# Kernel optimization log

Hardware: AMD Instinct MI355X
Metric: run time of the kernel (lower is better)

Reference implementation:

```python
import jax, jax.numpy as jnp
import numpy as np

IMG = 640
NUM_CLASSES = 80
MAX_MATCHES = 10  # == num_gt (required by the module's one-hot loop broadcast)
ALPHA = 0.5
BETA = 6.0
EPS = 1e-05
KEPS = 1e-07  # keras backend epsilon


def _make_anchor_points():
    pts = []
    for s in (8, 16, 32):
        n = IMG // s
        xs = (jnp.arange(n, dtype=jnp.float32) + 0.5) * s
        gx, gy = jnp.meshgrid(xs, xs, indexing='xy')
        pts.append(jnp.stack([gx, gy], axis=-1).reshape(-1, 2))
    return jnp.concatenate(pts, axis=0)  # [8400, 2]


def setup_inputs() -> dict:
    key = jax.random.key(0)
    ks = jax.random.split(key, 6)
    B, A, C, G = 32, 8400, NUM_CLASSES, 10
    anchors = _make_anchor_points()                                  # [A,2]
    scores = jax.random.uniform(ks[0], (B, A, C), dtype=jnp.float32)
    # predicted boxes roughly centered on anchors
    ctr = anchors[None] + 8.0 * jax.random.normal(ks[1], (B, A, 2), dtype=jnp.float32)
    wh = 8.0 + 56.0 * jax.random.uniform(ks[2], (B, A, 2), dtype=jnp.float32)
    decode_bboxes = jnp.concatenate([ctr - wh / 2, ctr + wh / 2], axis=-1)  # [B,A,4]
    # ground-truth boxes (xyxy within image)
    gmin = jax.random.uniform(ks[3], (B, G, 2), dtype=jnp.float32) * (IMG - 170.0)
    gwh = 20.0 + 150.0 * jax.random.uniform(ks[4], (B, G, 2), dtype=jnp.float32)
    gt_bboxes = jnp.concatenate([gmin, gmin + gwh], axis=-1)         # [B,G,4]
    gt_labels = jax.random.randint(ks[5], (B, G), 0, C, dtype=jnp.int32)
    gt_mask = jnp.ones((B, G, 1), dtype=bool)
    return {"scores": scores, "decode_bboxes": decode_bboxes, "anchors": anchors,
            "gt_labels": gt_labels, "gt_bboxes": gt_bboxes, "gt_mask": gt_mask}


def compute_ciou(b1, b2):
    # b1 [B,G,1,4], b2 [B,1,A,4] -> [B,G,A]
    x1a, y1a, x2a, y2a = (b1[..., i] for i in range(4))
    x1b, y1b, x2b, y2b = (b2[..., i] for i in range(4))
    w1 = x2a - x1a
    h1 = y2a - y1a + 1e-05
    w2 = x2b - x1b
    h2 = y2b - y1b + 1e-05
    inter = (jnp.maximum(jnp.minimum(x2a, x2b) - jnp.maximum(x1a, x1b), 0.0) *
             jnp.maximum(jnp.minimum(y2a, y2b) - jnp.maximum(y1a, y1b), 0.0))
    union = w1 * h1 + w2 * h2 - inter + 1e-05
    iou = inter / (union + 1e-05)
    cw = jnp.maximum(x2a, x2b) - jnp.minimum(x1a, x1b)
    ch = jnp.maximum(y2a, y2b) - jnp.minimum(y1a, y1b)
    c2 = cw ** 2 + ch ** 2 + KEPS
    rho2 = (((x1a + x2a) - (x1b + x2b)) / 2) ** 2 + (((y1a + y2a) - (y1b + y2b)) / 2) ** 2
    v = (4.0 / np.pi ** 2) * (jnp.arctan(w2 / h2) - jnp.arctan(w1 / h1)) ** 2
    alpha = v / (v - iou + (1.0 + KEPS))
    return iou - (rho2 / c2 + v * alpha)


def reference(scores, decode_bboxes, anchors, gt_labels, gt_bboxes, gt_mask):
    B, A, C = scores.shape
    G = gt_bboxes.shape[1]
    # per-gt class score for every anchor: [B,G,A]
    idx = jnp.broadcast_to(jnp.maximum(gt_labels, 0)[:, None, :], (B, A, G))
    bbox_scores = jnp.take_along_axis(scores, idx, axis=-1)          # [B,A,G]
    bbox_scores = jnp.transpose(bbox_scores, (0, 2, 1))              # [B,G,A]
    overlaps = compute_ciou(gt_bboxes[:, :, None, :], decode_bboxes[:, None, :, :])  # [B,G,A]
    align = jnp.power(bbox_scores, ALPHA) * jnp.power(overlaps, BETA)
    align = jnp.where(gt_mask, align, 0.0)
    # anchor center strictly inside gt box: [B,G,A]
    in_box = jnp.all((gt_bboxes[:, :, None, :2] < anchors) &
                     (gt_bboxes[:, :, None, 2:] > anchors), axis=-1)
    align = jnp.where(in_box, align, 0.0)
    cand_vals, cand_idxs = jax.lax.top_k(align, MAX_MATCHES)         # [B,G,K]
    cand_idxs = jnp.where(cand_vals > 0, cand_idxs, -1)
    # faithful to original loop: sum_k one_hot(cand_idxs[:, k], A)  -> sum over axis 1
    matched = jax.nn.one_hot(cand_idxs, A, dtype=overlaps.dtype).sum(axis=1)  # [B,K,A]==[B,G,A]
    overlaps = overlaps * matched
    gt_match = jnp.argmax(overlaps, axis=1).astype(jnp.int32)        # [B,A]
    match_mask = jnp.max(overlaps, axis=1) > 0                       # [B,A]
    bbox_labels = jnp.take_along_axis(
        gt_bboxes, jnp.broadcast_to(gt_match[:, :, None], (B, A, 4)), axis=1)  # [B,A,4]
    bbox_labels = jnp.where(match_mask[:, :, None], bbox_labels, -1.0)
    class_labels = jnp.take_along_axis(gt_labels, gt_match, axis=1)  # [B,A]
    class_labels = jnp.where(match_mask, class_labels, -1)
    class_labels = jax.nn.one_hot(class_labels, C, dtype=scores.dtype)  # [B,A,C]
    align = align * matched
    max_align = jnp.max(align, axis=-1, keepdims=True)               # [B,G,1]
    max_overlap = jnp.max(overlaps, axis=-1, keepdims=True)          # [B,G,1]
    norm_align = jnp.max(align * max_overlap / (max_align + EPS), axis=-2)  # [B,A]
    class_labels = class_labels * norm_align[:, :, None]
    fg_mask = (gt_match > -1).astype(jnp.float32)                    # [B,A]
    return (jax.lax.stop_gradient(bbox_labels.reshape(-1, A, 4)),
            jax.lax.stop_gradient(class_labels),
            jax.lax.stop_gradient(fg_mask))
```

## Files before the change

kernel.cpp:

```cpp
#include <hip/hip_runtime.h>
#include <math.h>

#define A_TOT 8400
#define NGT 10
#define NCLS 80
#define KTOP 10
#define NB_BATCH 32
#define CAP 1024

typedef unsigned int u32;
typedef unsigned long long u64;

struct GtP {
    float x1, y1, x2, y2;
    float area1;
    float at1;
    float sx, sy;
    int lab;
    int rawlab;
};

__device__ __forceinline__ void compute_pair(
    const GtP& g,
    float x1b, float y1b, float x2b, float y2b,
    float area2, float at2, float sxb, float syb,
    float ax, float ay, float score,
    float* ciou_out, float* align_out)
{
    float iw = fmaxf(fminf(g.x2, x2b) - fmaxf(g.x1, x1b), 0.0f);
    float ih = fmaxf(fminf(g.y2, y2b) - fmaxf(g.y1, y1b), 0.0f);
    float inter = iw * ih;
    float uni = g.area1 + area2 - inter + 1e-5f;
    float iou = inter / (uni + 1e-5f);
    float cw = fmaxf(g.x2, x2b) - fminf(g.x1, x1b);
    float ch = fmaxf(g.y2, y2b) - fminf(g.y1, y1b);
    float c2 = cw * cw + ch * ch + 1e-7f;
    float dx = (g.sx - sxb) * 0.5f;
    float dy = (g.sy - syb) * 0.5f;
    float rho2 = dx * dx + dy * dy;
    float dat = at2 - g.at1;
    float v = 0.40528473456935109f * (dat * dat);
    float alpha = v / (v - iou + 1.0000001f);
    float o = iou - (rho2 / c2 + v * alpha);
    *ciou_out = o;
    bool inb = (g.x1 < ax) && (g.y1 < ay) && (g.x2 > ax) && (g.y2 > ay);
    float o2 = o * o;
    float p6 = o2 * o2 * o2;
    *align_out = inb ? (sqrtf(score) * p6) : 0.0f;
}

__device__ __forceinline__ void load_gt(const float* gbox, const int* glab, int b, int g, GtP* out)
{
    const float* p = gbox + ((size_t)b * NGT + g) * 4;
    float x1 = p[0], y1 = p[1], x2 = p[2], y2 = p[3];
    out->x1 = x1; out->y1 = y1; out->x2 = x2; out->y2 = y2;
    float w1 = x2 - x1;
    float h1 = y2 - y1 + 1e-5f;
    out->area1 = w1 * h1;
    out->at1 = atanf(w1 / h1);
    out->sx = x1 + x2;
    out->sy = y1 + y2;
    int lb = glab[b * NGT + g];
    out->rawlab = lb;
    out->lab = lb > 0 ? lb : 0;
}

__global__ __launch_bounds__(256) void k_fill(float4* __restrict__ out, int* __restrict__ counters)
{
    const int NBv = 268800;
    const int NCv = 5644800;
    const int NTv = 5712000;
    int i = blockIdx.x * blockDim.x + threadIdx.x;
    if (i < NB_BATCH * NGT) counters[i] = 0;
    int stride = gridDim.x * blockDim.x;
    for (; i < NTv; i += stride) {
        float v = (i < NBv) ? -1.0f : (i < NCv ? 0.0f : 1.0f);
        out[i] = make_float4(v, v, v, v);
    }
}

__global__ __launch_bounds__(256) void k_align(
    const float* __restrict__ scores, const float* __restrict__ dec,
    const float* __restrict__ anch, const int* __restrict__ glab,
    const float* __restrict__ gbox,
    u64* __restrict__ entries, int* __restrict__ counters)
{
    __shared__ GtP sg[NGT];
    int b = blockIdx.y, tid = threadIdx.x;
    if (tid < NGT) load_gt(gbox, glab, b, tid, &sg[tid]);
    __syncthreads();

    int a = blockIdx.x * 256 + tid;
    if (a >= A_TOT) return;

    float4 bx = ((const float4*)dec)[(size_t)b * A_TOT + a];
    float x1b = bx.x, y1b = bx.y, x2b = bx.z, y2b = bx.w;
    float w2 = x2b - x1b;
    float h2 = y2b - y1b + 1e-5f;
    float area2 = w2 * h2;
    float at2 = atanf(w2 / h2);
    float sxb = x1b + x2b, syb = y1b + y2b;
    float2 ap = ((const float2*)anch)[a];
    const float* srow = scores + ((size_t)b * A_TOT + a) * NCLS;

    #pragma unroll
    for (int g = 0; g < NGT; ++g) {
        bool inb = (sg[g].x1 < ap.x) && (sg[g].y1 < ap.y) &&
                   (sg[g].x2 > ap.x) && (sg[g].y2 > ap.y);
        if (!inb) continue;
        float ci, al;
        compute_pair(sg[g], x1b, y1b, x2b, y2b, area2, at2, sxb, syb,
                     ap.x, ap.y, srow[sg[g].lab], &ci, &al);
        if (al > 0.0f) {
            int row = b * NGT + g;
            int pos = atomicAdd(&counters[row], 1);
            if (pos < CAP) {
                u64 key = ((u64)__float_as_uint(al) << 32) | (u32)(~(u32)a);
                entries[(size_t)row * CAP + pos] = key;
            }
        }
    }
}

__device__ __forceinline__ u64 shfl_xor_u64(u64 x, int m)
{
    u32 lo = (u32)x, hi = (u32)(x >> 32);
    lo = __shfl_xor(lo, m, 64);
    hi = __shfl_xor(hi, m, 64);
    return ((u64)hi << 32) | lo;
}

__global__ __launch_bounds__(64) void k_topk(
    const u64* __restrict__ entries, const int* __restrict__ counters,
    int* __restrict__ cidx)
{
    int row = blockIdx.x;
    int lane = threadIdx.x;
    int n = counters[row];
    if (n > CAP) n = CAP;
    const u64* e = entries + (size_t)row * CAP;

    u64 L[10];
    #pragma unroll
    for (int j = 0; j < 10; ++j) L[j] = 0ull;

    for (int i = lane; i < n; i += 64) {
        u64 key = e[i];
        if (key > L[9]) {
            L[9] = key;
            #pragma unroll
            for (int j = 9; j > 0; --j) {
                u64 x = L[j - 1], y = L[j];
                if (y > x) { L[j - 1] = y; L[j] = x; }
            }
        }
    }

    #pragma unroll
    for (int k = 0; k < KTOP; ++k) {
        u64 c = L[0];
        #pragma unroll
        for (int off = 1; off <= 32; off <<= 1) {
            u64 o = shfl_xor_u64(c, off);
            if (o > c) c = o;
        }
        if (c != 0ull && L[0] == c) {
            #pragma unroll
            for (int j = 0; j < 9; ++j) L[j] = L[j + 1];
            L[9] = 0ull;
        }
        if (lane == 0) {
            int idx = (int)(~(u32)(c & 0xFFFFFFFFu));
            cidx[row * KTOP + k] = (c != 0ull) ? idx : -1;
        }
    }
}

__global__ __launch_bounds__(128) void k_final(
    const float* __restrict__ scores, const float* __restrict__ dec,
    const float* __restrict__ anch, const int* __restrict__ glab,
    const float* __restrict__ gbox, const int* __restrict__ cidx,
    float* __restrict__ out_bbox, float* __restrict__ out_cls)
{
    __shared__ int cid[100];
    __shared__ GtP sg[NGT];
    __shared__ float aLS[NGT][100];
    __shared__ float oLS[NGT][100];
    __shared__ float Cg[NGT];
    int b = blockIdx.x, tid = threadIdx.x;

    if (tid < 100) cid[tid] = cidx[b * 100 + tid];
    if (tid < NGT) load_gt(gbox, glab, b, tid, &sg[tid]);
    __syncthreads();

    for (int t = tid; t < NGT * 100; t += 128) {
        int g = t / 100, e = t - g * 100;
        int a = cid[e];
        float ci = 0.0f, al = 0.0f;
        if (a >= 0) {
            float4 bx = ((const float4*)dec)[(size_t)b * A_TOT + a];
            float x1b = bx.x, y1b = bx.y, x2b = bx.z, y2b = bx.w;
            float w2 = x2b - x1b;
            float h2 = y2b - y1b + 1e-5f;
            float area2 = w2 * h2;
            float at2 = atanf(w2 / h2);
            float2 ap = ((const float2*)anch)[a];
            float s = scores[((size_t)b * A_TOT + a) * NCLS + sg[g].lab];
            compute_pair(sg[g], x1b, y1b, x2b, y2b, area2, at2,
                         x1b + x2b, y1b + y2b, ap.x, ap.y, s, &ci, &al);
        }
        oLS[g][e] = ci;
        aLS[g][e] = al;
    }
    __syncthreads();

    if (tid < NGT) {
        int j = tid;
        float mA = 0.0f, mO = 0.0f;
        for (int gp = 0; gp < NGT; ++gp) {
            int e = gp * NGT + j;
            int a = cid[e];
            if (a < 0) continue;
            int m = 0;
            for (int gq = 0; gq < NGT; ++gq) m += (cid[gq * NGT + j] == a);
            float fm = (float)m;
            mA = fmaxf(mA, aLS[j][e] * fm);
            mO = fmaxf(mO, oLS[j][e] * fm);
        }
        Cg[j] = mO / (mA + 1e-5f);
    }
    __syncthreads();

    if (tid < 100) {
        int e = tid, a = cid[e];
        if (a >= 0) {
            float best = -INFINITY;
            int bg = 0;
            float nrm = 0.0f;
            #pragma unroll
            for (int g = 0; g < NGT; ++g) {
                int m = 0;
                #pragma unroll
                for (int gq = 0; gq < NGT; ++gq) m += (cid[gq * NGT + g] == a);
                float fm = (float)m;
                float vo = oLS[g][e] * fm;
                if (vo > best) { best = vo; bg = g; }
                nrm = fmaxf(nrm, aLS[g][e] * fm * Cg[g]);
            }
            if (best > 0.0f) {
                float4 bb = make_float4(sg[bg].x1, sg[bg].y1, sg[bg].x2, sg[bg].y2);
                ((float4*)out_bbox)[(size_t)b * A_TOT + a] = bb;
                int rl = sg[bg].rawlab;
                if (rl >= 0 && rl < NCLS)
                    out_cls[((size_t)b * A_TOT + a) * NCLS + rl] = nrm;
            }
        }
    }
}

extern "C" void kernel_launch(void* const* d_in, const int* in_sizes, int n_in,
                              void* d_out, int out_size, void* d_ws, size_t ws_size,
                              hipStream_t stream)
{
    (void)in_sizes; (void)n_in; (void)out_size; (void)ws_size;
    const float* scores = (const float*)d_in[0];
    const float* dec    = (const float*)d_in[1];
    const float* anch   = (const float*)d_in[2];
    const int*   glab   = (const int*)d_in[3];
    const float* gbox   = (const float*)d_in[4];

    float* out      = (float*)d_out;
    float* out_bbox = out;
    float* out_cls  = out + (size_t)NB_BATCH * A_TOT * 4;

    int* counters = (int*)d_ws;
    u64* entries  = (u64*)((char*)d_ws + 4096);
    int* cidx     = (int*)((char*)d_ws + 4096 + (size_t)NB_BATCH * NGT * CAP * 8);

    k_fill <<<2048, 256, 0, stream>>>((float4*)d_out, counters);
    k_align<<<dim3(33, NB_BATCH), 256, 0, stream>>>(scores, dec, anch, glab, gbox, entries, counters);
    k_topk <<<NB_BATCH * NGT, 64, 0, stream>>>(entries, counters, cidx);
    k_final<<<NB_BATCH, 128, 0, stream>>>(scores, dec, anch, glab, gbox, cidx, out_bbox, out_cls);
}
```

Baseline: 178.6 us.

## Fuse output fill into align kernel, merge top-k into final, aggregate atomics

The output-fill loop moves into the align kernel, so one launch both writes the default output values and computes alignment candidates. The separate top-k kernel is folded into the final kernel, with one wavefront per ground-truth row running the selection and passing indices through shared memory. Per-lane atomicAdd calls are replaced by a wave-level ballot with a single leader atomic. This removes launches and intermediate global traffic, but the fill now runs on fewer threads and the final kernel uses larger 640-thread blocks over only 32 blocks.

New measurement: 178.4 us. Within noise of the previous version (-0.1%).

```diff
diff --git a/kernel.cpp b/kernel.cpp
--- a/kernel.cpp
+++ b/kernel.cpp
@@ -65,59 +65,75 @@
     out->lab = lb > 0 ? lb : 0;
 }
 
-__global__ __launch_bounds__(256) void k_fill(float4* __restrict__ out, int* __restrict__ counters)
-{
-    const int NBv = 268800;
-    const int NCv = 5644800;
-    const int NTv = 5712000;
-    int i = blockIdx.x * blockDim.x + threadIdx.x;
-    if (i < NB_BATCH * NGT) counters[i] = 0;
-    int stride = gridDim.x * blockDim.x;
-    for (; i < NTv; i += stride) {
-        float v = (i < NBv) ? -1.0f : (i < NCv ? 0.0f : 1.0f);
-        out[i] = make_float4(v, v, v, v);
-    }
-}
-
-__global__ __launch_bounds__(256) void k_align(
+__global__ __launch_bounds__(320) void k_zero(int* __restrict__ counters)
+{
+    counters[threadIdx.x] = 0;
+}
+
+__global__ __launch_bounds__(256) void k_alignfill(
     const float* __restrict__ scores, const float* __restrict__ dec,
     const float* __restrict__ anch, const int* __restrict__ glab,
     const float* __restrict__ gbox,
-    u64* __restrict__ entries, int* __restrict__ counters)
+    u64* __restrict__ entries, int* __restrict__ counters,
+    float4* __restrict__ outv)
 {
     __shared__ GtP sg[NGT];
     int b = blockIdx.y, tid = threadIdx.x;
     if (tid < NGT) load_gt(gbox, glab, b, tid, &sg[tid]);
     __syncthreads();
 
+    {
+        const int NBv = 268800;
+        const int NCv = 5644800;
+        const int NTv = 5712000;
+        int lin = (b * 33 + blockIdx.x) * 256 + tid;
+        const int stride = 33 * NB_BATCH * 256;
+        for (int i = lin; i < NTv; i += stride) {
+            float v = (i < NBv) ? -1.0f : (i < NCv ? 0.0f : 1.0f);
+            outv[i] = make_float4(v, v, v, v);
+        }
+    }
+
     int a = blockIdx.x * 256 + tid;
-    if (a >= A_TOT) return;
-
-    float4 bx = ((const float4*)dec)[(size_t)b * A_TOT + a];
+    bool valid = (a < A_TOT);
+    int asafe = valid ? a : 0;
+
+    float4 bx = ((const float4*)dec)[(size_t)b * A_TOT + asafe];
     float x1b = bx.x, y1b = bx.y, x2b = bx.z, y2b = bx.w;
     float w2 = x2b - x1b;
     float h2 = y2b - y1b + 1e-5f;
     float area2 = w2 * h2;
     float at2 = atanf(w2 / h2);
     float sxb = x1b + x2b, syb = y1b + y2b;
-    float2 ap = ((const float2*)anch)[a];
-    const float* srow = scores + ((size_t)b * A_TOT + a) * NCLS;
+    float2 ap = ((const float2*)anch)[asafe];
+    const float* srow = scores + ((size_t)b * A_TOT + asafe) * NCLS;
+    int lane = tid & 63;
 
     #pragma unroll
     for (int g = 0; g < NGT; ++g) {
-        bool inb = (sg[g].x1 < ap.x) && (sg[g].y1 < ap.y) &&
+        bool inb = valid &&
+                   (sg[g].x1 < ap.x) && (sg[g].y1 < ap.y) &&
                    (sg[g].x2 > ap.x) && (sg[g].y2 > ap.y);
-        if (!inb) continue;
-        float ci, al;
-        compute_pair(sg[g], x1b, y1b, x2b, y2b, area2, at2, sxb, syb,
-                     ap.x, ap.y, srow[sg[g].lab], &ci, &al);
-        if (al > 0.0f) {
-            int row = b * NGT + g;
-            int pos = atomicAdd(&counters[row], 1);
-            if (pos < CAP) {
-                u64 key = ((u64)__float_as_uint(al) << 32) | (u32)(~(u32)a);
-                entries[(size_t)row * CAP + pos] = key;
-            }
+        float al = 0.0f;
+        if (inb) {
+            float ci;
+            compute_pair(sg[g], x1b, y1b, x2b, y2b, area2, at2, sxb, syb,
+                         ap.x, ap.y, srow[sg[g].lab], &ci, &al);
+        }
+        bool pred = (al > 0.0f);
+        u64 mask = __ballot(pred);
+        if (mask == 0ull) continue;
+        int row = b * NGT + g;
+        int leader = __ffsll((long long)mask) - 1;
+        int cnt = __popcll(mask);
+        int prefix = __popcll(mask & ((1ull << lane) - 1ull));
+        int base = 0;
+        if (lane == leader) base = atomicAdd(&counters[row], cnt);
+        base = __shfl(base, leader, 64);
+        int pos = base + prefix;
+        if (pred && pos < CAP) {
+            u64 key = ((u64)__float_as_uint(al) << 32) | (u32)(~(u32)a);
+            entries[(size_t)row * CAP + pos] = key;
         }
     }
 }
@@ -130,56 +146,11 @@
     return ((u64)hi << 32) | lo;
 }
 
-__global__ __launch_bounds__(64) void k_topk(
-    const u64* __restrict__ entries, const int* __restrict__ counters,
-    int* __restrict__ cidx)
-{
-    int row = blockIdx.x;
-    int lane = threadIdx.x;
-    int n = counters[row];
-    if (n > CAP) n = CAP;
-    const u64* e = entries + (size_t)row * CAP;
-
-    u64 L[10];
-    #pragma unroll
-    for (int j = 0; j < 10; ++j) L[j] = 0ull;
-
-    for (int i = lane; i < n; i += 64) {
-        u64 key = e[i];
-        if (key > L[9]) {
-            L[9] = key;
-            #pragma unroll
-            for (int j = 9; j > 0; --j) {
-                u64 x = L[j - 1], y = L[j];
-                if (y > x) { L[j - 1] = y; L[j] = x; }
-            }
-        }
-    }
-
-    #pragma unroll
-    for (int k = 0; k < KTOP; ++k) {
-        u64 c = L[0];
-        #pragma unroll
-        for (int off = 1; off <= 32; off <<= 1) {
-            u64 o = shfl_xor_u64(c, off);
-            if (o > c) c = o;
-        }
-        if (c != 0ull && L[0] == c) {
-            #pragma unroll
-            for (int j = 0; j < 9; ++j) L[j] = L[j + 1];
-            L[9] = 0ull;
-        }
-        if (lane == 0) {
-            int idx = (int)(~(u32)(c & 0xFFFFFFFFu));
-            cidx[row * KTOP + k] = (c != 0ull) ? idx : -1;
-        }
-    }
-}
-
-__global__ __launch_bounds__(128) void k_final(
+__global__ __launch_bounds__(640) void k_sel(
     const float* __restrict__ scores, const float* __restrict__ dec,
     const float* __restrict__ anch, const int* __restrict__ glab,
-    const float* __restrict__ gbox, const int* __restrict__ cidx,
+    const float* __restrict__ gbox,
+    const u64* __restrict__ entries, const int* __restrict__ counters,
     float* __restrict__ out_bbox, float* __restrict__ out_cls)
 {
     __shared__ int cid[100];
@@ -188,12 +159,52 @@
     __shared__ float oLS[NGT][100];
     __shared__ float Cg[NGT];
     int b = blockIdx.x, tid = threadIdx.x;
-
-    if (tid < 100) cid[tid] = cidx[b * 100 + tid];
+    int wid = tid >> 6, lane = tid & 63;
+
     if (tid < NGT) load_gt(gbox, glab, b, tid, &sg[tid]);
-    __syncthreads();
-
-    for (int t = tid; t < NGT * 100; t += 128) {
+
+    {
+        int row = b * NGT + wid;
+        int n = counters[row];
+        if (n > CAP) n = CAP;
+        const u64* e = entries + (size_t)row * CAP;
+
+        u64 L[10];
+        #pragma unroll
+        for (int j = 0; j < 10; ++j) L[j] = 0ull;
+        for (int i = lane; i < n; i += 64) {
+            u64 key = e[i];
+            if (key > L[9]) {
+                L[9] = key;
+                #pragma unroll
+                for (int j = 9; j > 0; --j) {
+                    u64 x = L[j - 1], y = L[j];
+                    if (y > x) { L[j - 1] = y; L[j] = x; }
+                }
+            }
+        }
+        #pragma unroll
+        for (int k = 0; k < KTOP; ++k) {
+            u64 c = L[0];
+            #pragma unroll
+            for (int off = 1; off <= 32; off <<= 1) {
+                u64 o = shfl_xor_u64(c, off);
+                if (o > c) c = o;
+            }
+            if (c != 0ull && L[0] == c) {
+                #pragma unroll
+                for (int j = 0; j < 9; ++j) L[j] = L[j + 1];
+                L[9] = 0ull;
+            }
+            if (lane == 0) {
+                int idx = (int)(~(u32)(c & 0xFFFFFFFFu));
+                cid[wid * KTOP + k] = (c != 0ull) ? idx : -1;
+            }
+        }
+    }
+    __syncthreads();
+
+    for (int t = tid; t < NGT * 100; t += 640) {
         int g = t / 100, e = t - g * 100;
         int a = cid[e];
         float ci = 0.0f, al = 0.0f;
@@ -275,10 +286,10 @@
 
     int* counters = (int*)d_ws;
     u64* entries  = (u64*)((char*)d_ws + 4096);
-    int* cidx     = (int*)((char*)d_ws + 4096 + (size_t)NB_BATCH * NGT * CAP * 8);
-
-    k_fill <<<2048, 256, 0, stream>>>((float4*)d_out, counters);
-    k_align<<<dim3(33, NB_BATCH), 256, 0, stream>>>(scores, dec, anch, glab, gbox, entries, counters);
-    k_topk <<<NB_BATCH * NGT, 64, 0, stream>>>(entries, counters, cidx);
-    k_final<<<NB_BATCH, 128, 0, stream>>>(scores, dec, anch, glab, gbox, cidx, out_bbox, out_cls);
-}
+
+    k_zero     <<<1, 320, 0, stream>>>(counters);
+    k_alignfill<<<dim3(33, NB_BATCH), 256, 0, stream>>>(scores, dec, anch, glab, gbox,
+                                                        entries, counters, (float4*)d_out);
+    k_sel      <<<NB_BATCH, 640, 0, stream>>>(scores, dec, anch, glab, gbox,
+                                              entries, counters, out_bbox, out_cls);
+}
```
